# Performance work log

Hardware: AMD Instinct MI355X
Metric: run time of the kernel (lower is better)

The kernel has to match this reference:

```python
import jax, jax.numpy as jnp
import numpy as np

N = 20000      # nodes
E = 320000     # edges (before self-loops)
G = 64         # graphs in batch
IN = 128       # in_channels
HID = 64       # hidden_dim
NEG_SLOPE = 0.2


def setup_inputs() -> dict:
    key = jax.random.key(0)
    ks = jax.random.split(key, 20)
    def glorot(k, shape):
        fan = shape[0] + shape[-1]
        return jax.random.normal(k, shape, jnp.float32) * np.sqrt(2.0 / fan)
    inp = {
        'x': jax.random.normal(ks[0], (N, IN), jnp.float32),
        'edge_index': jax.random.randint(ks[1], (2, E), 0, N, jnp.int32),
        'batch': jnp.sort(jax.random.randint(ks[2], (N,), 0, G, jnp.int32)),
        # GAT layer 1: heads=4, out=64, concat=False
        'W1': glorot(ks[3], (IN, 4 * HID)),
        'as1': glorot(ks[4], (4, HID)),
        'ad1': glorot(ks[5], (4, HID)),
        'b1': jnp.zeros((HID,), jnp.float32),
        # GAT layer 2: heads=2, out=32, concat=False
        'W2': glorot(ks[6], (HID, 2 * (HID // 2))),
        'as2': glorot(ks[7], (2, HID // 2)),
        'ad2': glorot(ks[8], (2, HID // 2)),
        'b2': jnp.zeros((HID // 2,), jnp.float32),
        # continue head: 32->16->1
        'cW1': glorot(ks[9], (HID // 2, HID // 4)), 'cb1': jnp.zeros((HID // 4,), jnp.float32),
        'cW2': glorot(ks[10], (HID // 4, 1)), 'cb2': jnp.zeros((1,), jnp.float32),
        # halt head: 32->16->1
        'hW1': glorot(ks[11], (HID // 2, HID // 4)), 'hb1': jnp.zeros((HID // 4,), jnp.float32),
        'hW2': glorot(ks[12], (HID // 4, 1)), 'hb2': jnp.zeros((1,), jnp.float32),
    }
    return inp


def gat_layer(x, src, dst, W, att_src, att_dst, bias, heads, out_ch):
    # x: [N, Fin] -> h: [N, H, C]
    n = x.shape[0]
    h = (x @ W).reshape(n, heads, out_ch)
    a_src = jnp.einsum('nhc,hc->nh', h, att_src)   # [N, H]
    a_dst = jnp.einsum('nhc,hc->nh', h, att_dst)   # [N, H]
    e = jax.nn.leaky_relu(a_src[src] + a_dst[dst], NEG_SLOPE)   # [E', H]
    # segment softmax over incoming edges of each dst node
    m = jax.ops.segment_max(e, dst, num_segments=n)             # [N, H]
    ee = jnp.exp(e - m[dst])
    denom = jax.ops.segment_sum(ee, dst, num_segments=n)        # [N, H]
    alpha = ee / (denom[dst] + 1e-16)                           # [E', H]
    msg = h[src] * alpha[:, :, None]                            # [E', H, C]
    out = jax.ops.segment_sum(msg, dst, num_segments=n)         # [N, H, C]
    return out.mean(axis=1) + bias                              # concat=False -> head mean


def reference(x, edge_index, batch, W1, as1, ad1, b1, W2, as2, ad2, b2,
              cW1, cb1, cW2, cb2, hW1, hb1, hW2, hb2):
    n = x.shape[0]
    loop = jnp.arange(n, dtype=edge_index.dtype)
    src = jnp.concatenate([edge_index[0], loop])   # add self-loops (PyG default)
    dst = jnp.concatenate([edge_index[1], loop])

    h1 = jax.nn.relu(gat_layer(x, src, dst, W1, as1, ad1, b1, 4, HID))
    h2 = jax.nn.relu(gat_layer(h1, src, dst, W2, as2, ad2, b2, 2, HID // 2))

    # global mean pool per graph
    sums = jax.ops.segment_sum(h2, batch, num_segments=G)                 # [G, 32]
    cnt = jax.ops.segment_sum(jnp.ones((n,), h2.dtype), batch, num_segments=G)
    emb = sums / jnp.maximum(cnt, 1.0)[:, None]                           # [G, 32]

    cont = jax.nn.sigmoid(jax.nn.relu(emb @ cW1 + cb1) @ cW2 + cb2)       # [G, 1]
    halt = jax.nn.sigmoid(jax.nn.relu(emb @ hW1 + hb1) @ hW2 + hb2)       # [G, 1]
    return (halt, cont)
```

## Files before the change

kernel.cpp:

```cpp
#include <hip/hip_runtime.h>
#include <hip/hip_fp16.h>


#define G_GRAPHS 64

using half8   = __attribute__((ext_vector_type(8))) _Float16;
using half4v  = __attribute__((ext_vector_type(4))) _Float16;
using floatx4 = __attribute__((ext_vector_type(4))) float;
using floatx2 = __attribute__((ext_vector_type(2))) float;

__global__ __launch_bounds__(256) void zero_deg(int4* __restrict__ deg4, int n4)
{
    int i = blockIdx.x * 256 + threadIdx.x;
    if (i < n4) deg4[i] = int4{0, 0, 0, 0};
}

template<int K, int HPB, bool STORE_FP8, bool A_FP32, bool B_FP32>
__device__ __forceinline__ void gemm_att_tile(
        const void* __restrict__ A_v, const void* __restrict__ B_v,
        void* __restrict__ C_out, const float* __restrict__ att_s,
        const float* __restrict__ att_d, float* __restrict__ a_s,
        float* __restrict__ a_d, int M, int Ntot, int Htot,
        int row0, int col0, int by,
        _Float16 (*As)[K + 8], _Float16 (*Bt)[K + 8])
{
    constexpr int CPH = 64 / HPB;
    constexpr int NTH = 4 / HPB;
    const int tid = threadIdx.x;

    {
        int row = tid >> 2;
        int kc  = (tid & 3) * (K / 4);
        int gr  = row0 + row;
        #pragma unroll
        for (int i = 0; i < K / 32; i++) {
            half8 v = {};
            if (gr < M) {
                if constexpr (A_FP32) {
                    const float* Af = (const float*)A_v;
                    float4 f0 = *reinterpret_cast<const float4*>(&Af[(size_t)gr * K + kc + i * 8]);
                    float4 f1 = *reinterpret_cast<const float4*>(&Af[(size_t)gr * K + kc + i * 8 + 4]);
                    v[0] = (_Float16)f0.x; v[1] = (_Float16)f0.y;
                    v[2] = (_Float16)f0.z; v[3] = (_Float16)f0.w;
                    v[4] = (_Float16)f1.x; v[5] = (_Float16)f1.y;
                    v[6] = (_Float16)f1.z; v[7] = (_Float16)f1.w;
                } else {
                    const _Float16* Ah = (const _Float16*)A_v;
                    v = *reinterpret_cast<const half8*>(&Ah[(size_t)gr * K + kc + i * 8]);
                }
            }
            *reinterpret_cast<half8*>(&As[row][kc + i * 8]) = v;
        }
    }
    {
        #pragma unroll
        for (int i = 0; i < K / 16; i++) {
            int id = tid + 256 * i;
            int k  = id >> 4;
            int n4 = (id & 15) * 4;
            _Float16 b0, b1, b2, b3;
            if constexpr (B_FP32) {
                const float* Bf = (const float*)B_v;
                float4 f = *reinterpret_cast<const float4*>(&Bf[(size_t)k * Ntot + col0 + n4]);
                b0 = (_Float16)f.x; b1 = (_Float16)f.y;
                b2 = (_Float16)f.z; b3 = (_Float16)f.w;
            } else {
                const _Float16* Bh = (const _Float16*)B_v;
                half4v v = *reinterpret_cast<const half4v*>(&Bh[(size_t)k * Ntot + col0 + n4]);
                b0 = v[0]; b1 = v[1]; b2 = v[2]; b3 = v[3];
            }
            Bt[n4 + 0][k] = b0; Bt[n4 + 1][k] = b1;
            Bt[n4 + 2][k] = b2; Bt[n4 + 3][k] = b3;
        }
    }
    __syncthreads();

    const int wid  = tid >> 6;
    const int lane = tid & 63;
    const int r    = lane & 15;
    const int quad = lane >> 4;
    const int rw0  = wid * 16;

    floatx4 acc[4] = {};
    #pragma unroll
    for (int s = 0; s < K / 32; s++) {
        half8 af = *reinterpret_cast<const half8*>(&As[rw0 + r][s * 32 + quad * 8]);
        #pragma unroll
        for (int nt = 0; nt < 4; nt++) {
            half8 bf = *reinterpret_cast<const half8*>(&Bt[nt * 16 + r][s * 32 + quad * 8]);
            acc[nt] = __builtin_amdgcn_mfma_f32_16x16x32_f16(af, bf, acc[nt], 0, 0, 0);
        }
    }

    float ps[HPB][4], pd[HPB][4];
    #pragma unroll
    for (int hl = 0; hl < HPB; hl++)
        #pragma unroll
        for (int reg = 0; reg < 4; reg++) { ps[hl][reg] = 0.f; pd[hl][reg] = 0.f; }

    #pragma unroll
    for (int nt = 0; nt < 4; nt++) {
        int hl = nt / NTH;
        int cl = (nt % NTH) * 16 + r;
        int hglob = by * HPB + hl;
        float ws = att_s[hglob * CPH + cl];
        float wd = att_d[hglob * CPH + cl];
        #pragma unroll
        for (int reg = 0; reg < 4; reg++) {
            ps[hl][reg] += acc[nt][reg] * ws;
            pd[hl][reg] += acc[nt][reg] * wd;
        }
    }
    #pragma unroll
    for (int off = 1; off < 16; off <<= 1)
        #pragma unroll
        for (int hl = 0; hl < HPB; hl++)
            #pragma unroll
            for (int reg = 0; reg < 4; reg++) {
                ps[hl][reg] += __shfl_xor(ps[hl][reg], off);
                pd[hl][reg] += __shfl_xor(pd[hl][reg], off);
            }
    if (r == 0) {
        #pragma unroll
        for (int reg = 0; reg < 4; reg++) {
            int gr = row0 + rw0 + quad * 4 + reg;
            if (gr < M) {
                #pragma unroll
                for (int hl = 0; hl < HPB; hl++) {
                    int hglob = by * HPB + hl;
                    a_s[gr * Htot + hglob] = ps[hl][reg];
                    a_d[gr * Htot + hglob] = pd[hl][reg];
                }
            }
        }
    }

    if constexpr (STORE_FP8) {
        __syncthreads();
        unsigned char (*lds8)[80] = reinterpret_cast<unsigned char(*)[80]>(&As[0][0]);
        #pragma unroll
        for (int nt = 0; nt < 4; nt++) {
            #pragma unroll
            for (int reg = 0; reg < 4; reg++) {
                int wv = __builtin_amdgcn_cvt_pk_fp8_f32(
                    acc[nt][reg], acc[nt][reg], 0, false);
                lds8[rw0 + quad * 4 + reg][nt * 16 + r] = (unsigned char)(wv & 0xFF);
            }
        }
        __syncthreads();
        unsigned char* C8 = (unsigned char*)C_out;
        int row = tid >> 2;
        int c16 = (tid & 3) * 16;
        int gr  = row0 + row;
        if (gr < M) {
            int4 v = *reinterpret_cast<const int4*>(&lds8[row][c16]);
            *reinterpret_cast<int4*>(&C8[(size_t)gr * Ntot + col0 + c16]) = v;
        }
    } else {
        _Float16* Ch = (_Float16*)C_out;
        #pragma unroll
        for (int nt = 0; nt < 4; nt++) {
            #pragma unroll
            for (int reg = 0; reg < 4; reg++) {
                int gr = row0 + rw0 + quad * 4 + reg;
                if (gr < M)
                    Ch[(size_t)gr * Ntot + col0 + nt * 16 + r] = (_Float16)acc[nt][reg];
            }
        }
    }
}

__global__ __launch_bounds__(256) void count_gemm1(
        const int* __restrict__ ei, int* __restrict__ deg,
        int* __restrict__ col_ell, int E0, int Etot, int eb,
        const float* __restrict__ A, const float* __restrict__ B,
        void* __restrict__ C_out, const float* __restrict__ att_s,
        const float* __restrict__ att_d, float* __restrict__ a_s,
        float* __restrict__ a_d, int M, int mb)
{
    __shared__ _Float16 As[64][136];
    __shared__ _Float16 Bt[64][136];

    if ((int)blockIdx.x < eb) {
        int idx = blockIdx.x * 256 + threadIdx.x;
        if (idx < Etot) {
            int src = (idx < E0) ? ei[idx]      : (idx - E0);
            int dst = (idx < E0) ? ei[E0 + idx] : (idx - E0);
            int slot = atomicAdd(&deg[dst], 1);
            if (slot < 64)
                col_ell[(size_t)dst * 64 + slot] = src;
        }
        return;
    }
    const int bx   = (int)blockIdx.x - eb;
    const int row0 = (bx % mb) * 64;
    const int by   = bx / mb;
    gemm_att_tile<128, 1, true, true, true>(
        A, B, C_out, att_s, att_d, a_s, a_d,
        M, 256, 4, row0, by * 64, by, As, Bt);
}

__global__ __launch_bounds__(256) void gemm2_kernel(
        const _Float16* __restrict__ A, const float* __restrict__ B,
        _Float16* __restrict__ Ch, const float* __restrict__ att_s,
        const float* __restrict__ att_d, float* __restrict__ a_s,
        float* __restrict__ a_d, int M)
{
    __shared__ _Float16 As[64][72];
    __shared__ _Float16 Bt[64][72];
    gemm_att_tile<64, 2, false, false, true>(
        A, B, Ch, att_s, att_d, a_s, a_d,
        M, 64, 2, blockIdx.x * 64, 0, 0, As, Bt);
}

__device__ inline void facc4_h(float* a, float2 raw, float p) {
    __half2 h0 = *reinterpret_cast<__half2*>(&raw.x);
    __half2 h1 = *reinterpret_cast<__half2*>(&raw.y);
    float2 f0 = __half22float2(h0), f1 = __half22float2(h1);
    a[0] += p * f0.x; a[1] += p * f0.y; a[2] += p * f1.x; a[3] += p * f1.y;
}
__device__ inline void facc4_8(float* a, unsigned int w, float p) {
    floatx2 lo = __builtin_amdgcn_cvt_pk_f32_fp8((int)w, false);
    floatx2 hi = __builtin_amdgcn_cvt_pk_f32_fp8((int)w, true);
    a[0] += p * lo[0]; a[1] += p * lo[1]; a[2] += p * hi[0]; a[3] += p * hi[1];
}
__device__ inline void facc8_8(float* a, uint2 w, float p) {
    facc4_8(a,     w.x, p);
    facc4_8(a + 4, w.y, p);
}

template<int H, int C, bool OUT_HALF, bool FEAT_FP8>
__device__ void gat_general(
        int d, int lo, int degc, const int* __restrict__ colidx,
        const void* __restrict__ hfeat_v, const float* __restrict__ a_s,
        const float* __restrict__ a_d, const float* __restrict__ bias,
        void* __restrict__ out_v, int N, float* p_wave)
{
    if (d >= N) return;
    constexpr int FV = (H * C) / 64;
    const int lane = threadIdx.x & 63;
    const int hi = lo + degc;
    const __half* hfeat = (const __half*)hfeat_v;
    const unsigned char* ffeat = (const unsigned char*)hfeat_v;
    const int h_lane = (lane * FV) / C;

    float adp[H];
    #pragma unroll
    for (int h = 0; h < H; h++) adp[h] = a_d[d * H + h];
    float lh[H];
    #pragma unroll
    for (int h = 0; h < H; h++) lh[h] = 0.f;
    float acc[FV];
    #pragma unroll
    for (int v = 0; v < FV; v++) acc[v] = 0.f;

    float mh[H];
    #pragma unroll
    for (int h = 0; h < H; h++) mh[h] = -3.0e38f;
    for (int i = lo + lane; i < hi; i += 64) {
        int s = colidx[i];
        #pragma unroll
        for (int h = 0; h < H; h++) {
            float v = a_s[s * H + h] + adp[h];
            v = (v > 0.f) ? v : 0.2f * v;
            mh[h] = fmaxf(mh[h], v);
        }
    }
    #pragma unroll
    for (int off = 1; off < 64; off <<= 1)
        #pragma unroll
        for (int h = 0; h < H; h++)
            mh[h] = fmaxf(mh[h], __shfl_xor(mh[h], off));

    for (int base = lo; base < hi; base += 64) {
        int i = base + lane;
        int s = 0;
        if (i < hi) {
            s = colidx[i];
            #pragma unroll
            for (int h = 0; h < H; h++) {
                float v = a_s[s * H + h] + adp[h];
                v = (v > 0.f) ? v : 0.2f * v;
                float p = __expf(v - mh[h]);
                lh[h] += p;
                p_wave[(i - base) * H + h] = p;
            }
        }
        int cnt = min(64, hi - base);
        for (int j = 0; j < cnt; j++) {
            int s_j = __shfl(s, j);
            float pj = p_wave[j * H + h_lane];
            if constexpr (FV == 4 && FEAT_FP8) {
                unsigned int raw = *reinterpret_cast<const unsigned int*>(
                    ffeat + (size_t)s_j * (H * C) + lane * 4);
                facc4_8(acc, raw, pj);
            } else if constexpr (FV == 4) {
                float2 raw = *reinterpret_cast<const float2*>(
                    hfeat + (size_t)s_j * (H * C) + lane * 4);
                facc4_h(acc, raw, pj);
            } else {
                acc[0] += pj * __half2float(hfeat[(size_t)s_j * (H * C) + lane]);
            }
        }
    }
    #pragma unroll
    for (int off = 1; off < 64; off <<= 1)
        #pragma unroll
        for (int h = 0; h < H; h++)
            lh[h] += __shfl_xor(lh[h], off);

    float lsel = lh[0];
    #pragma unroll
    for (int h = 1; h < H; h++) if (h_lane == h) lsel = lh[h];
    const float inv = 1.0f / (lsel + 1e-16f);

    if constexpr (FV == 4) {
        float vx = acc[0] * inv, vy = acc[1] * inv,
              vz = acc[2] * inv, vw = acc[3] * inv;
        vx += __shfl_xor(vx, 16); vy += __shfl_xor(vy, 16);
        vz += __shfl_xor(vz, 16); vw += __shfl_xor(vw, 16);
        vx += __shfl_xor(vx, 32); vy += __shfl_xor(vy, 32);
        vz += __shfl_xor(vz, 32); vw += __shfl_xor(vw, 32);
        if (lane < 16) {
            float4 bv = *reinterpret_cast<const float4*>(&bias[lane * 4]);
            float ox = fmaxf(0.25f * vx + bv.x, 0.f);
            float oy = fmaxf(0.25f * vy + bv.y, 0.f);
            float oz = fmaxf(0.25f * vz + bv.z, 0.f);
            float ow = fmaxf(0.25f * vw + bv.w, 0.f);
            if constexpr (OUT_HALF) {
                half4v hv = { (_Float16)ox, (_Float16)oy, (_Float16)oz, (_Float16)ow };
                *reinterpret_cast<half4v*>((_Float16*)out_v + (size_t)d * C + lane * 4) = hv;
            } else {
                float4 o = make_float4(ox, oy, oz, ow);
                *reinterpret_cast<float4*>((float*)out_v + (size_t)d * C + lane * 4) = o;
            }
        }
    } else {
        float v = acc[0] * inv;
        v += __shfl_xor(v, 32);
        if (lane < 32) {
            float o = fmaxf(0.5f * v + bias[lane], 0.f);
            if constexpr (OUT_HALF)
                ((_Float16*)out_v)[(size_t)d * C + lane] = (_Float16)o;
            else
                ((float*)out_v)[(size_t)d * C + lane] = o;
        }
    }
}

template<int H, int C, bool OUT_HALF, bool FEAT_FP8>
__global__ __launch_bounds__(256) void gat_dst(
        const int* __restrict__ degv, const int* __restrict__ col_ell,
        const void* __restrict__ hfeat_v, const float* __restrict__ a_s,
        const float* __restrict__ a_d, const float* __restrict__ bias,
        void* __restrict__ out_v, int N)
{
    const int wid  = threadIdx.x >> 6;
    const int lane = threadIdx.x & 63;
    const int nw   = lane >> 5;
    const int l32  = lane & 31;

    __shared__ float p_sh[4][64 * H];

    const int d  = blockIdx.x * 8 + wid * 2 + nw;
    const bool nodeok = (d < N);
    const int lo = d * 64;

    int degc = 0;
    if (nodeok) degc = min(degv[d], 64);
    const int degA = __shfl(degc, 0);
    const int degB = __shfl(degc, 32);
    const bool fast = (degA <= 32) && (degB <= 32);

    if (fast) {
        const __half* hfeat = (const __half*)hfeat_v;
        const unsigned char* ffeat = (const unsigned char*)hfeat_v;

        float adp[H];
        #pragma unroll
        for (int h = 0; h < H; h++) adp[h] = nodeok ? a_d[d * H + h] : 0.f;

        int s = 0;
        float lh[H];
        #pragma unroll
        for (int h = 0; h < H; h++) lh[h] = 0.f;
        const bool valid = nodeok && (l32 < degc);
        if (valid) {
            s = col_ell[lo + l32];
            if constexpr (H == 4) {
                float4 av = *reinterpret_cast<const float4*>(&a_s[s * 4]);
                float ev[4] = {av.x + adp[0], av.y + adp[1],
                               av.z + adp[2], av.w + adp[3]};
                #pragma unroll
                for (int h = 0; h < 4; h++) {
                    float e = (ev[h] > 0.f) ? ev[h] : 0.2f * ev[h];
                    float p = __expf(e);
                    lh[h] = p;
                    p_sh[wid][nw * 32 * H + l32 * H + h] = p;
                }
            } else {
                float2 av = *reinterpret_cast<const float2*>(&a_s[s * 2]);
                float ev[2] = {av.x + adp[0], av.y + adp[1]};
                #pragma unroll
                for (int h = 0; h < 2; h++) {
                    float e = (ev[h] > 0.f) ? ev[h] : 0.2f * ev[h];
                    float p = __expf(e);
                    lh[h] = p;
                    p_sh[wid][nw * 32 * H + l32 * H + h] = p;
                }
            }
        }
        #pragma unroll
        for (int off = 1; off < 32; off <<= 1)
            #pragma unroll
            for (int h = 0; h < H; h++)
                lh[h] += __shfl_xor(lh[h], off);

        const int sbase = nw * 32;

        if constexpr (H == 4) {
            const int hl = l32 >> 3;
            float a0[8] = {}, a1[8] = {};
            int j = 0;
            for (; j + 8 <= degc; j += 8) {
                uint2 raw[8]; float pw[8];
                #pragma unroll
                for (int u = 0; u < 8; u++) {
                    int sj = __shfl(s, sbase + j + u);
                    pw[u]  = p_sh[wid][nw * 128 + (j + u) * 4 + hl];
                    raw[u] = *reinterpret_cast<const uint2*>(
                        ffeat + (size_t)sj * 256 + l32 * 8);
                }
                #pragma unroll
                for (int u = 0; u < 8; u++)
                    facc8_8((u & 1) ? a1 : a0, raw[u], pw[u]);
            }
            for (; j < degc; j++) {
                int sj = __shfl(s, sbase + j);
                float pw = p_sh[wid][nw * 128 + j * 4 + hl];
                uint2 raw = *reinterpret_cast<const uint2*>(
                    ffeat + (size_t)sj * 256 + l32 * 8);
                facc8_8(a0, raw, pw);
            }
            #pragma unroll
            for (int k = 0; k < 8; k++) a0[k] += a1[k];

            float lsel = lh[0];
            #pragma unroll
            for (int h = 1; h < 4; h++) if (hl == h) lsel = lh[h];
            float inv = 1.0f / (lsel + 1e-16f);
            #pragma unroll
            for (int k = 0; k < 8; k++) {
                float v = a0[k] * inv;
                v += __shfl_xor(v, 8);
                v += __shfl_xor(v, 16);
                a0[k] = v;
            }
            if (nodeok && l32 < 8) {
                float4 b0 = *reinterpret_cast<const float4*>(&bias[l32 * 8]);
                float4 b1 = *reinterpret_cast<const float4*>(&bias[l32 * 8 + 4]);
                float bb[8] = {b0.x, b0.y, b0.z, b0.w, b1.x, b1.y, b1.z, b1.w};
                half8 hv;
                #pragma unroll
                for (int k = 0; k < 8; k++)
                    hv[k] = (_Float16)fmaxf(0.25f * a0[k] + bb[k], 0.f);
                *reinterpret_cast<half8*>((_Float16*)out_v + (size_t)d * 64 + l32 * 8) = hv;
            }
        } else {
            const int q   = l32 >> 4;
            const int l16 = l32 & 15;
            const int hl2 = l16 >> 3;
            float a0[4] = {}, a1[4] = {};
            int j = 0;
            for (; j + 8 <= degc; j += 8) {
                float2 raw[4]; float pw[4];
                #pragma unroll
                for (int u = 0; u < 4; u++) {
                    int je = j + 2 * u + q;
                    int sj = __shfl(s, sbase + je);
                    pw[u]  = p_sh[wid][nw * 64 + je * 2 + hl2];
                    raw[u] = *reinterpret_cast<const float2*>(
                        (const _Float16*)hfeat + (size_t)sj * 64 + l16 * 4);
                }
                #pragma unroll
                for (int u = 0; u < 4; u++)
                    facc4_h((u & 1) ? a1 : a0, raw[u], pw[u]);
            }
            for (int jr = j + q; jr < degc; jr += 2) {
                int sj = __shfl(s, sbase + jr);
                float pw = p_sh[wid][nw * 64 + jr * 2 + hl2];
                float2 raw = *reinterpret_cast<const float2*>(
                    (const _Float16*)hfeat + (size_t)sj * 64 + l16 * 4);
                facc4_h(a0, raw, pw);
            }
            #pragma unroll
            for (int k = 0; k < 4; k++) {
                a0[k] += a1[k];
                a0[k] += __shfl_xor(a0[k], 16);
            }
            float lsel = (hl2 == 0) ? lh[0] : lh[1];
            float inv = 1.0f / (lsel + 1e-16f);
            #pragma unroll
            for (int k = 0; k < 4; k++) {
                float v = a0[k] * inv;
                v += __shfl_xor(v, 8);
                a0[k] = v;
            }
            if (nodeok && l32 < 8) {
                float4 bb = *reinterpret_cast<const float4*>(&bias[l32 * 4]);
                float4 o;
                o.x = fmaxf(0.5f * a0[0] + bb.x, 0.f);
                o.y = fmaxf(0.5f * a0[1] + bb.y, 0.f);
                o.z = fmaxf(0.5f * a0[2] + bb.z, 0.f);
                o.w = fmaxf(0.5f * a0[3] + bb.w, 0.f);
                *reinterpret_cast<float4*>((float*)out_v + (size_t)d * 32 + l32 * 4) = o;
            }
        }
        return;
    }

    const int dA = blockIdx.x * 8 + wid * 2;
    gat_general<H, C, OUT_HALF, FEAT_FP8>(
        dA, dA * 64, __shfl(degc, 0), col_ell,
        hfeat_v, a_s, a_d, bias, out_v, N, p_sh[wid]);
    gat_general<H, C, OUT_HALF, FEAT_FP8>(
        dA + 1, (dA + 1) * 64, __shfl(degc, 32), col_ell,
        hfeat_v, a_s, a_d, bias, out_v, N, p_sh[wid]);
}

__global__ __launch_bounds__(256) void pool_heads(
        const float* __restrict__ h2, const int* __restrict__ batch,
        const float* __restrict__ cW1, const float* __restrict__ cb1,
        const float* __restrict__ cW2, const float* __restrict__ cb2,
        const float* __restrict__ hW1, const float* __restrict__ hb1,
        const float* __restrict__ hW2, const float* __restrict__ hb2,
        float* __restrict__ out, int N)
{
    const int g = blockIdx.x;
    const int c = threadIdx.x & 31;
    const int r = threadIdx.x >> 5;

    __shared__ int bounds[2];
    __shared__ float red[8][32];
    __shared__ float emb_s[32];
    __shared__ float hidden[32];

    if (threadIdx.x < 2) {
        int target = g + (int)threadIdx.x;
        int lo = 0, hi = N;
        while (lo < hi) {
            int mid = (lo + hi) >> 1;
            if (batch[mid] < target) lo = mid + 1; else hi = mid;
        }
        bounds[threadIdx.x] = lo;
    }
    __syncthreads();
    const int lo = bounds[0], hi = bounds[1];

    float acc = 0.f;
    for (int n = lo + r; n < hi; n += 8)
        acc += h2[(size_t)n * 32 + c];
    red[r][c] = acc;
    __syncthreads();
    if (r == 0) {
        float s = 0.f;
        #pragma unroll
        for (int i = 0; i < 8; i++) s += red[i][c];
        emb_s[c] = s / fmaxf((float)(hi - lo), 1.0f);
    }
    __syncthreads();

    if (threadIdx.x < 32) {
        int j = threadIdx.x & 15;
        bool is_halt = threadIdx.x >= 16;
        const float* w1v = is_halt ? hW1 : cW1;
        const float* b1v = is_halt ? hb1 : cb1;
        const float* w2v = is_halt ? hW2 : cW2;
        float s = b1v[j];
        #pragma unroll
        for (int cc = 0; cc < 32; cc++) s += emb_s[cc] * w1v[cc * 16 + j];
        hidden[threadIdx.x] = fmaxf(s, 0.f) * w2v[j];
    }
    __syncthreads();
    if (threadIdx.x == 0) {
        float sc = cb2[0], sh = hb2[0];
        #pragma unroll
        for (int i = 0; i < 16; i++) { sc += hidden[i]; sh += hidden[16 + i]; }
        out[g]            = 1.0f / (1.0f + __expf(-sh));
        out[G_GRAPHS + g] = 1.0f / (1.0f + __expf(-sc));
    }
}

extern "C" void kernel_launch(void* const* d_in, const int* in_sizes, int n_in,
                              void* d_out, int out_size, void* d_ws, size_t ws_size,
                              hipStream_t stream)
{
    const float* x   = (const float*)d_in[0];
    const int*   ei  = (const int*)  d_in[1];
    const int*   bat = (const int*)  d_in[2];
    const float* W1  = (const float*)d_in[3];
    const float* as1 = (const float*)d_in[4];
    const float* ad1 = (const float*)d_in[5];
    const float* b1  = (const float*)d_in[6];
    const float* W2  = (const float*)d_in[7];
    const float* as2 = (const float*)d_in[8];
    const float* ad2 = (const float*)d_in[9];
    const float* b2  = (const float*)d_in[10];
    const float* cW1 = (const float*)d_in[11];
    const float* cb1 = (const float*)d_in[12];
    const float* cW2 = (const float*)d_in[13];
    const float* cb2 = (const float*)d_in[14];
    const float* hW1 = (const float*)d_in[15];
    const float* hb1 = (const float*)d_in[16];
    const float* hW2 = (const float*)d_in[17];
    const float* hb2 = (const float*)d_in[18];

    const int N    = in_sizes[2];
    const int E0   = in_sizes[1] / 2;
    const int Etot = E0 + N;
    const int IN   = in_sizes[0] / N;

    float* w = (float*)d_ws;
    size_t o = 0;
    unsigned char* h1pre_f8 = (unsigned char*)(w + o); o += (size_t)N * 64;
    _Float16* h1_h    = (_Float16*)(w + o); o += (size_t)N * 32;
    _Float16* h2pre_h = (_Float16*)(w + o); o += (size_t)N * 32;
    float* a_s1  = w + o; o += (size_t)N * 4;
    float* a_d1  = w + o; o += (size_t)N * 4;
    float* a_s2  = w + o; o += (size_t)N * 2;
    float* a_d2  = w + o; o += (size_t)N * 2;
    float* h2    = w + o; o += (size_t)N * 32;
    int* deg     = (int*)(w + o); o += ((size_t)N + 3) & ~(size_t)3;
    int* col_ell = (int*)(w + o); o += (size_t)N * 64;
    (void)ws_size; (void)n_in; (void)out_size; (void)IN;

    const dim3 blk(256);
    const int eb  = (Etot + 255) / 256;
    const int nb8 = (N + 7) / 8;
    const int mb  = (N + 63) / 64;

    const int n4 = (N + 3) / 4;
    zero_deg<<<(n4 + 255) / 256, blk, 0, stream>>>((int4*)deg, n4);

    count_gemm1<<<eb + mb * 4, blk, 0, stream>>>(
        ei, deg, col_ell, E0, Etot, eb,
        x, W1, h1pre_f8, as1, ad1, a_s1, a_d1, N, mb);

    gat_dst<4, 64, true, true><<<nb8, blk, 0, stream>>>(
        deg, col_ell, h1pre_f8, a_s1, a_d1, b1, h1_h, N);

    gemm2_kernel<<<mb, blk, 0, stream>>>(
        h1_h, W2, h2pre_h, as2, ad2, a_s2, a_d2, N);
    gat_dst<2, 32, false, false><<<nb8, blk, 0, stream>>>(
        deg, col_ell, h2pre_h, a_s2, a_d2, b2, h2, N);

    pool_heads<<<G_GRAPHS, blk, 0, stream>>>(
        h2, bat, cW1, cb1, cW2, cb2, hW1, hb1, hW2, hb2, (float*)d_out, N);
}
```

Before: 106.1 us.

## Fuse layer-1 GAT aggregation with layer-2 linear transform and attention scores

Merges the layer-1 aggregation kernel and the separate gemm2 kernel into one kernel. Each wave computes a node's h1 row in shared memory, multiplies it by a per-block transposed fp16 copy of W2, and writes h2pre plus the layer-2 attention scalars directly. This drops one launch and the h1 round trip through global memory. In exchange, every block reloads and transposes W2, the small GEMM runs on scalar FMAs instead of the tiled matrix path, and LDS use per block goes up.

```diff
diff --git a/kernel.cpp b/kernel.cpp
--- a/kernel.cpp
+++ b/kernel.cpp
@@ -198,19 +198,6 @@
     gemm_att_tile<128, 1, true, true, true>(
         A, B, C_out, att_s, att_d, a_s, a_d,
         M, 256, 4, row0, by * 64, by, As, Bt);
-}
-
-__global__ __launch_bounds__(256) void gemm2_kernel(
-        const _Float16* __restrict__ A, const float* __restrict__ B,
-        _Float16* __restrict__ Ch, const float* __restrict__ att_s,
-        const float* __restrict__ att_d, float* __restrict__ a_s,
-        float* __restrict__ a_d, int M)
-{
-    __shared__ _Float16 As[64][72];
-    __shared__ _Float16 Bt[64][72];
-    gemm_att_tile<64, 2, false, false, true>(
-        A, B, Ch, att_s, att_d, a_s, a_d,
-        M, 64, 2, blockIdx.x * 64, 0, 0, As, Bt);
 }
 
 __device__ inline void facc4_h(float* a, float2 raw, float p) {
@@ -374,7 +361,6 @@
 
     if (fast) {
         const __half* hfeat = (const __half*)hfeat_v;
-        const unsigned char* ffeat = (const unsigned char*)hfeat_v;
 
         float adp[H];
         #pragma unroll
@@ -387,27 +373,14 @@
         const bool valid = nodeok && (l32 < degc);
         if (valid) {
             s = col_ell[lo + l32];
-            if constexpr (H == 4) {
-                float4 av = *reinterpret_cast<const float4*>(&a_s[s * 4]);
-                float ev[4] = {av.x + adp[0], av.y + adp[1],
-                               av.z + adp[2], av.w + adp[3]};
-                #pragma unroll
-                for (int h = 0; h < 4; h++) {
-                    float e = (ev[h] > 0.f) ? ev[h] : 0.2f * ev[h];
-                    float p = __expf(e);
-                    lh[h] = p;
-                    p_sh[wid][nw * 32 * H + l32 * H + h] = p;
-                }
-            } else {
-                float2 av = *reinterpret_cast<const float2*>(&a_s[s * 2]);
-                float ev[2] = {av.x + adp[0], av.y + adp[1]};
-                #pragma unroll
-                for (int h = 0; h < 2; h++) {
-                    float e = (ev[h] > 0.f) ? ev[h] : 0.2f * ev[h];
-                    float p = __expf(e);
-                    lh[h] = p;
-                    p_sh[wid][nw * 32 * H + l32 * H + h] = p;
-                }
+            float2 av = *reinterpret_cast<const float2*>(&a_s[s * 2]);
+            float ev[2] = {av.x + adp[0], av.y + adp[1]};
+            #pragma unroll
+            for (int h = 0; h < 2; h++) {
+                float e = (ev[h] > 0.f) ? ev[h] : 0.2f * ev[h];
+                float p = __expf(e);
+                lh[h] = p;
+                p_sh[wid][nw * 32 * H + l32 * H + h] = p;
             }
         }
         #pragma unroll
@@ -418,103 +391,53 @@
 
         const int sbase = nw * 32;
 
-        if constexpr (H == 4) {
-            const int hl = l32 >> 3;
-            float a0[8] = {}, a1[8] = {};
-            int j = 0;
-            for (; j + 8 <= degc; j += 8) {
-                uint2 raw[8]; float pw[8];
-                #pragma unroll
-                for (int u = 0; u < 8; u++) {
-                    int sj = __shfl(s, sbase + j + u);
-                    pw[u]  = p_sh[wid][nw * 128 + (j + u) * 4 + hl];
-                    raw[u] = *reinterpret_cast<const uint2*>(
-                        ffeat + (size_t)sj * 256 + l32 * 8);
-                }
-                #pragma unroll
-                for (int u = 0; u < 8; u++)
-                    facc8_8((u & 1) ? a1 : a0, raw[u], pw[u]);
-            }
-            for (; j < degc; j++) {
-                int sj = __shfl(s, sbase + j);
-                float pw = p_sh[wid][nw * 128 + j * 4 + hl];
-                uint2 raw = *reinterpret_cast<const uint2*>(
-                    ffeat + (size_t)sj * 256 + l32 * 8);
-                facc8_8(a0, raw, pw);
-            }
-            #pragma unroll
-            for (int k = 0; k < 8; k++) a0[k] += a1[k];
-
-            float lsel = lh[0];
-            #pragma unroll
-            for (int h = 1; h < 4; h++) if (hl == h) lsel = lh[h];
-            float inv = 1.0f / (lsel + 1e-16f);
-            #pragma unroll
-            for (int k = 0; k < 8; k++) {
-                float v = a0[k] * inv;
-                v += __shfl_xor(v, 8);
-                v += __shfl_xor(v, 16);
-                a0[k] = v;
-            }
-            if (nodeok && l32 < 8) {
-                float4 b0 = *reinterpret_cast<const float4*>(&bias[l32 * 8]);
-                float4 b1 = *reinterpret_cast<const float4*>(&bias[l32 * 8 + 4]);
-                float bb[8] = {b0.x, b0.y, b0.z, b0.w, b1.x, b1.y, b1.z, b1.w};
-                half8 hv;
-                #pragma unroll
-                for (int k = 0; k < 8; k++)
-                    hv[k] = (_Float16)fmaxf(0.25f * a0[k] + bb[k], 0.f);
-                *reinterpret_cast<half8*>((_Float16*)out_v + (size_t)d * 64 + l32 * 8) = hv;
-            }
-        } else {
-            const int q   = l32 >> 4;
-            const int l16 = l32 & 15;
-            const int hl2 = l16 >> 3;
-            float a0[4] = {}, a1[4] = {};
-            int j = 0;
-            for (; j + 8 <= degc; j += 8) {
-                float2 raw[4]; float pw[4];
-                #pragma unroll
-                for (int u = 0; u < 4; u++) {
-                    int je = j + 2 * u + q;
-                    int sj = __shfl(s, sbase + je);
-                    pw[u]  = p_sh[wid][nw * 64 + je * 2 + hl2];
-                    raw[u] = *reinterpret_cast<const float2*>(
-                        (const _Float16*)hfeat + (size_t)sj * 64 + l16 * 4);
-                }
-                #pragma unroll
-                for (int u = 0; u < 4; u++)
-                    facc4_h((u & 1) ? a1 : a0, raw[u], pw[u]);
-            }
-            for (int jr = j + q; jr < degc; jr += 2) {
-                int sj = __shfl(s, sbase + jr);
-                float pw = p_sh[wid][nw * 64 + jr * 2 + hl2];
-                float2 raw = *reinterpret_cast<const float2*>(
+        const int q   = l32 >> 4;
+        const int l16 = l32 & 15;
+        const int hl2 = l16 >> 3;
+        float a0[4] = {}, a1[4] = {};
+        int j = 0;
+        for (; j + 8 <= degc; j += 8) {
+            float2 raw[4]; float pw[4];
+            #pragma unroll
+            for (int u = 0; u < 4; u++) {
+                int je = j + 2 * u + q;
+                int sj = __shfl(s, sbase + je);
+                pw[u]  = p_sh[wid][nw * 64 + je * 2 + hl2];
+                raw[u] = *reinterpret_cast<const float2*>(
                     (const _Float16*)hfeat + (size_t)sj * 64 + l16 * 4);
-                facc4_h(a0, raw, pw);
-            }
-            #pragma unroll
-            for (int k = 0; k < 4; k++) {
-                a0[k] += a1[k];
-                a0[k] += __shfl_xor(a0[k], 16);
-            }
-            float lsel = (hl2 == 0) ? lh[0] : lh[1];
-            float inv = 1.0f / (lsel + 1e-16f);
-            #pragma unroll
-            for (int k = 0; k < 4; k++) {
-                float v = a0[k] * inv;
-                v += __shfl_xor(v, 8);
-                a0[k] = v;
-            }
-            if (nodeok && l32 < 8) {
-                float4 bb = *reinterpret_cast<const float4*>(&bias[l32 * 4]);
-                float4 o;
-                o.x = fmaxf(0.5f * a0[0] + bb.x, 0.f);
-                o.y = fmaxf(0.5f * a0[1] + bb.y, 0.f);
-                o.z = fmaxf(0.5f * a0[2] + bb.z, 0.f);
-                o.w = fmaxf(0.5f * a0[3] + bb.w, 0.f);
-                *reinterpret_cast<float4*>((float*)out_v + (size_t)d * 32 + l32 * 4) = o;
-            }
+            }
+            #pragma unroll
+            for (int u = 0; u < 4; u++)
+                facc4_h((u & 1) ? a1 : a0, raw[u], pw[u]);
+        }
+        for (int jr = j + q; jr < degc; jr += 2) {
+            int sj = __shfl(s, sbase + jr);
+            float pw = p_sh[wid][nw * 64 + jr * 2 + hl2];
+            float2 raw = *reinterpret_cast<const float2*>(
+                (const _Float16*)hfeat + (size_t)sj * 64 + l16 * 4);
+            facc4_h(a0, raw, pw);
+        }
+        #pragma unroll
+        for (int k = 0; k < 4; k++) {
+            a0[k] += a1[k];
+            a0[k] += __shfl_xor(a0[k], 16);
+        }
+        float lsel = (hl2 == 0) ? lh[0] : lh[1];
+        float inv = 1.0f / (lsel + 1e-16f);
+        #pragma unroll
+        for (int k = 0; k < 4; k++) {
+            float v = a0[k] * inv;
+            v += __shfl_xor(v, 8);
+            a0[k] = v;
+        }
+        if (nodeok && l32 < 8) {
+            float4 bb = *reinterpret_cast<const float4*>(&bias[l32 * 4]);
+            float4 o;
+            o.x = fmaxf(0.5f * a0[0] + bb.x, 0.f);
+            o.y = fmaxf(0.5f * a0[1] + bb.y, 0.f);
+            o.z = fmaxf(0.5f * a0[2] + bb.z, 0.f);
+            o.w = fmaxf(0.5f * a0[3] + bb.w, 0.f);
+            *reinterpret_cast<float4*>((float*)out_v + (size_t)d * 32 + l32 * 4) = o;
         }
         return;
     }
@@ -526,6 +449,289 @@
     gat_general<H, C, OUT_HALF, FEAT_FP8>(
         dA + 1, (dA + 1) * 64, __shfl(degc, 32), col_ell,
         hfeat_v, a_s, a_d, bias, out_v, N, p_sh[wid]);
+}
+
+__device__ void gat1_general(
+        int d, int lo, int degc, const int* __restrict__ colidx,
+        const unsigned char* __restrict__ ffeat,
+        const float* __restrict__ a_s, const float* __restrict__ a_d,
+        const float* __restrict__ bias, int N, float* p_wave,
+        const _Float16 (*W2t)[72],
+        const float* __restrict__ as2, const float* __restrict__ ad2,
+        _Float16* __restrict__ h2pre,
+        float* __restrict__ a_s2, float* __restrict__ a_d2)
+{
+    if (d >= N) return;
+    const int lane = threadIdx.x & 63;
+    const int hi = lo + degc;
+    const int h_lane = lane >> 4;
+
+    float adp[4];
+    #pragma unroll
+    for (int h = 0; h < 4; h++) adp[h] = a_d[d * 4 + h];
+    float lh[4];
+    #pragma unroll
+    for (int h = 0; h < 4; h++) lh[h] = 0.f;
+    float acc[4];
+    #pragma unroll
+    for (int v = 0; v < 4; v++) acc[v] = 0.f;
+
+    float mh[4];
+    #pragma unroll
+    for (int h = 0; h < 4; h++) mh[h] = -3.0e38f;
+    for (int i = lo + lane; i < hi; i += 64) {
+        int s = colidx[i];
+        #pragma unroll
+        for (int h = 0; h < 4; h++) {
+            float v = a_s[s * 4 + h] + adp[h];
+            v = (v > 0.f) ? v : 0.2f * v;
+            mh[h] = fmaxf(mh[h], v);
+        }
+    }
+    #pragma unroll
+    for (int off = 1; off < 64; off <<= 1)
+        #pragma unroll
+        for (int h = 0; h < 4; h++)
+            mh[h] = fmaxf(mh[h], __shfl_xor(mh[h], off));
+
+    for (int base = lo; base < hi; base += 64) {
+        int i = base + lane;
+        int s = 0;
+        if (i < hi) {
+            s = colidx[i];
+            #pragma unroll
+            for (int h = 0; h < 4; h++) {
+                float v = a_s[s * 4 + h] + adp[h];
+                v = (v > 0.f) ? v : 0.2f * v;
+                float p = __expf(v - mh[h]);
+                lh[h] += p;
+                p_wave[(i - base) * 4 + h] = p;
+            }
+        }
+        int cnt = min(64, hi - base);
+        for (int j = 0; j < cnt; j++) {
+            int s_j = __shfl(s, j);
+            float pj = p_wave[j * 4 + h_lane];
+            unsigned int raw = *reinterpret_cast<const unsigned int*>(
+                ffeat + (size_t)s_j * 256 + lane * 4);
+            facc4_8(acc, raw, pj);
+        }
+    }
+    #pragma unroll
+    for (int off = 1; off < 64; off <<= 1)
+        #pragma unroll
+        for (int h = 0; h < 4; h++)
+            lh[h] += __shfl_xor(lh[h], off);
+
+    float lsel = lh[0];
+    #pragma unroll
+    for (int h = 1; h < 4; h++) if (h_lane == h) lsel = lh[h];
+    const float inv = 1.0f / (lsel + 1e-16f);
+
+    float vx = acc[0] * inv, vy = acc[1] * inv,
+          vz = acc[2] * inv, vw = acc[3] * inv;
+    vx += __shfl_xor(vx, 16); vy += __shfl_xor(vy, 16);
+    vz += __shfl_xor(vz, 16); vw += __shfl_xor(vw, 16);
+    vx += __shfl_xor(vx, 32); vy += __shfl_xor(vy, 32);
+    vz += __shfl_xor(vz, 32); vw += __shfl_xor(vw, 32);
+    if (lane < 16) {
+        float4 bv = *reinterpret_cast<const float4*>(&bias[lane * 4]);
+        p_wave[lane * 4 + 0] = (float)(_Float16)fmaxf(0.25f * vx + bv.x, 0.f);
+        p_wave[lane * 4 + 1] = (float)(_Float16)fmaxf(0.25f * vy + bv.y, 0.f);
+        p_wave[lane * 4 + 2] = (float)(_Float16)fmaxf(0.25f * vz + bv.z, 0.f);
+        p_wave[lane * 4 + 3] = (float)(_Float16)fmaxf(0.25f * vw + bv.w, 0.f);
+    }
+
+    float ga = 0.f;
+    #pragma unroll
+    for (int kb = 0; kb < 64; kb += 8) {
+        half8 wv = *reinterpret_cast<const half8*>(&W2t[lane][kb]);
+        float4 hA = *reinterpret_cast<const float4*>(&p_wave[kb]);
+        float4 hB = *reinterpret_cast<const float4*>(&p_wave[kb + 4]);
+        ga += hA.x * (float)wv[0] + hA.y * (float)wv[1]
+            + hA.z * (float)wv[2] + hA.w * (float)wv[3]
+            + hB.x * (float)wv[4] + hB.y * (float)wv[5]
+            + hB.z * (float)wv[6] + hB.w * (float)wv[7];
+    }
+    float ps = ga * as2[lane];
+    float pd = ga * ad2[lane];
+    #pragma unroll
+    for (int off = 1; off < 32; off <<= 1) {
+        ps += __shfl_xor(ps, off);
+        pd += __shfl_xor(pd, off);
+    }
+    h2pre[(size_t)d * 64 + lane] = (_Float16)ga;
+    if ((lane & 31) == 0) {
+        int h = lane >> 5;
+        a_s2[d * 2 + h] = ps;
+        a_d2[d * 2 + h] = pd;
+    }
+}
+
+__global__ __launch_bounds__(256) void gat1_fused(
+        const int* __restrict__ degv, const int* __restrict__ col_ell,
+        const unsigned char* __restrict__ ffeat,
+        const float* __restrict__ a_s, const float* __restrict__ a_d,
+        const float* __restrict__ bias,
+        const float* __restrict__ W2,
+        const float* __restrict__ as2, const float* __restrict__ ad2,
+        _Float16* __restrict__ h2pre,
+        float* __restrict__ a_s2, float* __restrict__ a_d2,
+        int N)
+{
+    __shared__ float p_sh[4][256];
+    __shared__ _Float16 W2t[64][72];
+
+    {
+        int t  = threadIdx.x;
+        int k  = t >> 2;
+        int cb = (t & 3) * 16;
+        #pragma unroll
+        for (int i = 0; i < 4; i++) {
+            float4 f = *reinterpret_cast<const float4*>(&W2[k * 64 + cb + i * 4]);
+            W2t[cb + i * 4 + 0][k] = (_Float16)f.x;
+            W2t[cb + i * 4 + 1][k] = (_Float16)f.y;
+            W2t[cb + i * 4 + 2][k] = (_Float16)f.z;
+            W2t[cb + i * 4 + 3][k] = (_Float16)f.w;
+        }
+    }
+    __syncthreads();
+
+    const int wid  = threadIdx.x >> 6;
+    const int lane = threadIdx.x & 63;
+    const int nw   = lane >> 5;
+    const int l32  = lane & 31;
+    float* psw = p_sh[wid];
+
+    const int d  = blockIdx.x * 8 + wid * 2 + nw;
+    const bool nodeok = (d < N);
+    const int lo = d * 64;
+
+    int degc = 0;
+    if (nodeok) degc = min(degv[d], 64);
+    const int degA = __shfl(degc, 0);
+    const int degB = __shfl(degc, 32);
+    const bool fast = (degA <= 32) && (degB <= 32);
+
+    if (fast) {
+        float adp[4];
+        #pragma unroll
+        for (int h = 0; h < 4; h++) adp[h] = nodeok ? a_d[d * 4 + h] : 0.f;
+
+        int s = 0;
+        float lh[4];
+        #pragma unroll
+        for (int h = 0; h < 4; h++) lh[h] = 0.f;
+        const bool valid = nodeok && (l32 < degc);
+        if (valid) {
+            s = col_ell[lo + l32];
+            float4 av = *reinterpret_cast<const float4*>(&a_s[s * 4]);
+            float ev[4] = {av.x + adp[0], av.y + adp[1],
+                           av.z + adp[2], av.w + adp[3]};
+            #pragma unroll
+            for (int h = 0; h < 4; h++) {
+                float e = (ev[h] > 0.f) ? ev[h] : 0.2f * ev[h];
+                float p = __expf(e);
+                lh[h] = p;
+                psw[nw * 128 + l32 * 4 + h] = p;
+            }
+        }
+        #pragma unroll
+        for (int off = 1; off < 32; off <<= 1)
+            #pragma unroll
+            for (int h = 0; h < 4; h++)
+                lh[h] += __shfl_xor(lh[h], off);
+
+        const int sbase = nw * 32;
+
+        const int hl = l32 >> 3;
+        float a0[8] = {}, a1[8] = {};
+        int j = 0;
+        for (; j + 8 <= degc; j += 8) {
+            uint2 raw[8]; float pw[8];
+            #pragma unroll
+            for (int u = 0; u < 8; u++) {
+                int sj = __shfl(s, sbase + j + u);
+                pw[u]  = psw[nw * 128 + (j + u) * 4 + hl];
+                raw[u] = *reinterpret_cast<const uint2*>(
+                    ffeat + (size_t)sj * 256 + l32 * 8);
+            }
+            #pragma unroll
+            for (int u = 0; u < 8; u++)
+                facc8_8((u & 1) ? a1 : a0, raw[u], pw[u]);
+        }
+        for (; j < degc; j++) {
+            int sj = __shfl(s, sbase + j);
+            float pw = psw[nw * 128 + j * 4 + hl];
+            uint2 raw = *reinterpret_cast<const uint2*>(
+                ffeat + (size_t)sj * 256 + l32 * 8);
+            facc8_8(a0, raw, pw);
+        }
+        #pragma unroll
+        for (int k = 0; k < 8; k++) a0[k] += a1[k];
+
+        float lsel = lh[0];
+        #pragma unroll
+        for (int h = 1; h < 4; h++) if (hl == h) lsel = lh[h];
+        float inv = 1.0f / (lsel + 1e-16f);
+        #pragma unroll
+        for (int k = 0; k < 8; k++) {
+            float v = a0[k] * inv;
+            v += __shfl_xor(v, 8);
+            v += __shfl_xor(v, 16);
+            a0[k] = v;
+        }
+
+        float* h1row = psw + nw * 64;
+        if (l32 < 8) {
+            float4 b0 = *reinterpret_cast<const float4*>(&bias[l32 * 8]);
+            float4 b1 = *reinterpret_cast<const float4*>(&bias[l32 * 8 + 4]);
+            float bb[8] = {b0.x, b0.y, b0.z, b0.w, b1.x, b1.y, b1.z, b1.w};
+            #pragma unroll
+            for (int k = 0; k < 8; k++)
+                h1row[l32 * 8 + k] =
+                    (float)(_Float16)fmaxf(0.25f * a0[k] + bb[k], 0.f);
+        }
+
+        float ac0 = 0.f, ac1 = 0.f;
+        #pragma unroll
+        for (int kb = 0; kb < 64; kb += 8) {
+            half8 w0 = *reinterpret_cast<const half8*>(&W2t[l32][kb]);
+            half8 w1 = *reinterpret_cast<const half8*>(&W2t[32 + l32][kb]);
+            float4 hA = *reinterpret_cast<const float4*>(&h1row[kb]);
+            float4 hB = *reinterpret_cast<const float4*>(&h1row[kb + 4]);
+            ac0 += hA.x * (float)w0[0] + hA.y * (float)w0[1]
+                 + hA.z * (float)w0[2] + hA.w * (float)w0[3]
+                 + hB.x * (float)w0[4] + hB.y * (float)w0[5]
+                 + hB.z * (float)w0[6] + hB.w * (float)w0[7];
+            ac1 += hA.x * (float)w1[0] + hA.y * (float)w1[1]
+                 + hA.z * (float)w1[2] + hA.w * (float)w1[3]
+                 + hB.x * (float)w1[4] + hB.y * (float)w1[5]
+                 + hB.z * (float)w1[6] + hB.w * (float)w1[7];
+        }
+        float ps0 = ac0 * as2[l32],      pd0 = ac0 * ad2[l32];
+        float ps1 = ac1 * as2[32 + l32], pd1 = ac1 * ad2[32 + l32];
+        #pragma unroll
+        for (int off = 1; off < 32; off <<= 1) {
+            ps0 += __shfl_xor(ps0, off); pd0 += __shfl_xor(pd0, off);
+            ps1 += __shfl_xor(ps1, off); pd1 += __shfl_xor(pd1, off);
+        }
+        if (nodeok) {
+            h2pre[(size_t)d * 64 + l32]      = (_Float16)ac0;
+            h2pre[(size_t)d * 64 + 32 + l32] = (_Float16)ac1;
+            if (l32 == 0) {
+                a_s2[d * 2 + 0] = ps0; a_s2[d * 2 + 1] = ps1;
+                a_d2[d * 2 + 0] = pd0; a_d2[d * 2 + 1] = pd1;
+            }
+        }
+        return;
+    }
+
+    const int dA = blockIdx.x * 8 + wid * 2;
+    gat1_general(dA,     dA * 64,       __shfl(degc, 0),  col_ell, ffeat,
+                 a_s, a_d, bias, N, psw, W2t, as2, ad2, h2pre, a_s2, a_d2);
+    gat1_general(dA + 1, (dA + 1) * 64, __shfl(degc, 32), col_ell, ffeat,
+                 a_s, a_d, bias, N, psw, W2t, as2, ad2, h2pre, a_s2, a_d2);
 }
 
 __global__ __launch_bounds__(256) void pool_heads(
@@ -618,12 +824,10 @@
     const int N    = in_sizes[2];
     const int E0   = in_sizes[1] / 2;
     const int Etot = E0 + N;
-    const int IN   = in_sizes[0] / N;
 
     float* w = (float*)d_ws;
     size_t o = 0;
     unsigned char* h1pre_f8 = (unsigned char*)(w + o); o += (size_t)N * 64;
-    _Float16* h1_h    = (_Float16*)(w + o); o += (size_t)N * 32;
     _Float16* h2pre_h = (_Float16*)(w + o); o += (size_t)N * 32;
     float* a_s1  = w + o; o += (size_t)N * 4;
     float* a_d1  = w + o; o += (size_t)N * 4;
@@ -632,7 +836,7 @@
     float* h2    = w + o; o += (size_t)N * 32;
     int* deg     = (int*)(w + o); o += ((size_t)N + 3) & ~(size_t)3;
     int* col_ell = (int*)(w + o); o += (size_t)N * 64;
-    (void)ws_size; (void)n_in; (void)out_size; (void)IN;
+    (void)ws_size; (void)n_in; (void)out_size;
 
     const dim3 blk(256);
     const int eb  = (Etot + 255) / 256;
@@ -646,11 +850,10 @@
         ei, deg, col_ell, E0, Etot, eb,
         x, W1, h1pre_f8, as1, ad1, a_s1, a_d1, N, mb);
 
-    gat_dst<4, 64, true, true><<<nb8, blk, 0, stream>>>(
-        deg, col_ell, h1pre_f8, a_s1, a_d1, b1, h1_h, N);
-
-    gemm2_kernel<<<mb, blk, 0, stream>>>(
-        h1_h, W2, h2pre_h, as2, ad2, a_s2, a_d2, N);
+    gat1_fused<<<nb8, blk, 0, stream>>>(
+        deg, col_ell, h1pre_f8, a_s1, a_d1, b1,
+        W2, as2, ad2, h2pre_h, a_s2, a_d2, N);
+
     gat_dst<2, 32, false, false><<<nb8, blk, 0, stream>>>(
         deg, col_ell, h2pre_h, a_s2, a_d2, b2, h2, N);
 
```

New measurement: 109.2 us. 1.03x slower.
